# Optimization experiments

Measured on AMD Instinct MI355X. Metric: run time of the kernel, lower is better.

The kernel has to match this reference:

```python
import jax, jax.numpy as jnp
import numpy as np

EPS = 1e-5  # torch BatchNorm1d / LayerNorm default eps
B, S, CTX, C, H = 64, 31, 2048, 512, 8  # S must be num_particles+1 = 31
DH = C // H


def layernorm(x, g, b):
    mu = x.mean(-1, keepdims=True)
    var = x.var(-1, keepdims=True)
    return (x - mu) / jnp.sqrt(var + EPS) * g + b


def setup_inputs() -> dict:
    key = jax.random.key(0)
    ks = jax.random.split(key, 16)
    w = lambda k, shape: jax.random.normal(k, shape, jnp.float32) * 0.02
    return {
        "queries": jax.random.normal(ks[0], (B, S, C), jnp.float32),
        "contexts": jax.random.normal(ks[1], (B, CTX, C), jnp.float32),
        # SelfAttention params (BatchNorm1d(C) in training mode, q/k/v no bias, out with bias)
        "sa_bn_g": jnp.ones((C,), jnp.float32),
        "sa_bn_b": jnp.zeros((C,), jnp.float32),
        "sa_q_w": w(ks[2], (C, C)),
        "sa_k_w": w(ks[3], (C, C)),
        "sa_v_w": w(ks[4], (C, C)),
        "sa_out_w": w(ks[5], (C, C)),
        "sa_out_b": jnp.zeros((C,), jnp.float32),
        "sa_pre_g": jnp.ones((S * S,), jnp.float32),  # BatchNorm1d(961) on energy
        "sa_pre_b": jnp.zeros((S * S,), jnp.float32),
        # Cross Attention params (LayerNorm on queries, q/k/v no bias, out with bias)
        "ca_ln_g": jnp.ones((C,), jnp.float32),
        "ca_ln_b": jnp.zeros((C,), jnp.float32),
        "ca_q_w": w(ks[6], (C, C)),
        "ca_k_w": w(ks[7], (C, C)),
        "ca_v_w": w(ks[8], (C, C)),
        "ca_out_w": w(ks[9], (C, C)),
        "ca_out_b": jnp.zeros((C,), jnp.float32),
        # FFN: LN -> SiLU -> Linear(C,2C,no bias) -> LN -> SiLU -> Linear(2C,C,no bias)
        "ff_ln1_g": jnp.ones((C,), jnp.float32),
        "ff_ln1_b": jnp.zeros((C,), jnp.float32),
        "ff_w1": w(ks[10], (2 * C, C)),
        "ff_ln2_g": jnp.ones((2 * C,), jnp.float32),
        "ff_ln2_b": jnp.zeros((2 * C,), jnp.float32),
        "ff_w2": w(ks[11], (C, 2 * C)),
    }


def reference(queries, contexts, sa_bn_g, sa_bn_b, sa_q_w, sa_k_w, sa_v_w,
              sa_out_w, sa_out_b, sa_pre_g, sa_pre_b, ca_ln_g, ca_ln_b,
              ca_q_w, ca_k_w, ca_v_w, ca_out_w, ca_out_b, ff_ln1_g, ff_ln1_b,
              ff_w1, ff_ln2_g, ff_ln2_b, ff_w2):
    scale = jnp.sqrt(jnp.asarray(C, queries.dtype))

    # ---- SelfAttention (normalization='Batch', training-mode batch stats) ----
    mu = queries.mean(axis=(0, 1))            # per-channel over (B, S)
    var = queries.var(axis=(0, 1))
    xn = (queries - mu) / jnp.sqrt(var + EPS) * sa_bn_g + sa_bn_b
    q = jnp.einsum('bsc,oc->bso', xn, sa_q_w).reshape(B, S, H, DH)
    k = jnp.einsum('bsc,oc->bso', xn, sa_k_w).reshape(B, S, H, DH)
    v = jnp.einsum('bsc,oc->bso', xn, sa_v_w).reshape(B, S, H, DH)
    energy = jnp.einsum('nqhc,nkhc->nhqk', q, k)          # (B,H,S,S)
    # pre-softmax BatchNorm1d over channels = flattened (q,k) positions, batch dims = (B, H)
    e = energy.reshape(B, H, S * S)                        # (B,H,S*S)
    mu2 = e.mean(axis=(0, 1))
    var2 = e.var(axis=(0, 1))
    en = (e - mu2) / jnp.sqrt(var2 + EPS) * sa_pre_g + sa_pre_b
    energy_post = en.reshape(B, H, S, S)
    attn = jax.nn.softmax(energy_post / scale, axis=-1)
    o = jnp.einsum('nhql,nlhc->nqhc', attn, v).reshape(B, S, C)
    o = jnp.einsum('bsc,oc->bso', o, sa_out_w) + sa_out_b
    x_sa = o + queries                                     # residual

    # ---- Cross Attention (LayerNorm on queries pre-projection) ----
    qn = layernorm(x_sa, ca_ln_g, ca_ln_b)
    q2 = jnp.einsum('bsc,oc->bso', qn, ca_q_w).reshape(B, S, H, DH)
    k2 = jnp.einsum('btc,oc->bto', contexts, ca_k_w).reshape(B, CTX, H, DH)
    v2 = jnp.einsum('btc,oc->bto', contexts, ca_v_w).reshape(B, CTX, H, DH)
    energy2 = jnp.einsum('nqhc,nkhc->nhqk', q2, k2)        # (B,H,S,CTX)
    attn2 = jax.nn.softmax(energy2 / scale, axis=-1)
    o2 = jnp.einsum('nhql,nlhc->nqhc', attn2, v2).reshape(B, S, C)
    o2 = jnp.einsum('bsc,oc->bso', o2, ca_out_w) + ca_out_b
    x_ca = o2 + x_sa                                       # residual (queries_pre)

    # ---- FFN: LN -> SiLU -> Linear -> LN -> SiLU -> Linear, + residual ----
    h = jax.nn.silu(layernorm(x_ca, ff_ln1_g, ff_ln1_b))
    h = jnp.einsum('bsc,oc->bso', h, ff_w1)                # (B,S,2C)
    h = jax.nn.silu(layernorm(h, ff_ln2_g, ff_ln2_b))
    h = jnp.einsum('bsc,oc->bso', h, ff_w2)                # (B,S,C)
    out = x_ca + h                                         # dropout p=0.0 -> identity
    return out, energy2
```

## Files before the change

### kernel.cpp

```cpp
#include <hip/hip_runtime.h>
#include <hip/hip_bf16.h>
#include <cstdint>
#include <cstddef>

using u16 = unsigned short;
typedef short short8 __attribute__((ext_vector_type(8)));
typedef short short4v __attribute__((ext_vector_type(4)));
typedef float f32x4  __attribute__((ext_vector_type(4)));

#define DEV static __device__ __forceinline__

DEV float b2f(u16 u){ union{ unsigned i; float f; } v; v.i = ((unsigned)u)<<16; return v.f; }
DEV u16 f2b(float f){
  unsigned i = __builtin_bit_cast(unsigned, f);
  unsigned r = (i + 0x7FFFu + ((i>>16)&1u)) >> 16;
  return (u16)r;
}
DEV f32x4 mfma16(short8 a, short8 b, f32x4 c){
  return __builtin_amdgcn_mfma_f32_16x16x32_bf16(a, b, c, 0, 0, 0);
}

constexpr int Bn=64, Sn=31, Tn=2048, Cn=512, Hn=8;
constexpr int Rn=Bn*Sn;
constexpr int BHn=Bn*Hn;
constexpr int HRn=Hn*Sn;
constexpr float EPSf=1e-5f;
constexpr float INV_SCALE=0.04419417382415922f;

__global__ void k_badorder(float* out){
  if(threadIdx.x==0) out[0]=2000.f;
}

__global__ __launch_bounds__(256) void k_cvt(const float* __restrict__ in,
    u16* __restrict__ out, int n8){
  int i = blockIdx.x*256 + threadIdx.x;
  if(i>=n8) return;
  f32x4 a=*(const f32x4*)&in[(size_t)i*8];
  f32x4 b=*(const f32x4*)&in[(size_t)i*8+4];
  short8 o;
  #pragma unroll
  for(int j=0;j<4;++j){ o[j]=(short)f2b(a[j]); o[4+j]=(short)f2b(b[j]); }
  *(short8*)&out[(size_t)i*8]=o;
}

__global__ __launch_bounds__(256) void k_bn1_partial(const float* __restrict__ q,
    float* __restrict__ ps, float* __restrict__ psq){
  int c = blockIdx.x*256 + threadIdx.x;
  int r0 = blockIdx.y*124;
  float s=0.f, sq=0.f;
  for(int r=r0; r<r0+124; ++r){ float v=q[(size_t)r*Cn+c]; s+=v; sq+=v*v; }
  ps [blockIdx.y*Cn+c]=s;
  psq[blockIdx.y*Cn+c]=sq;
}
__global__ __launch_bounds__(512) void k_bn1_final(const float* __restrict__ ps,
    const float* __restrict__ psq, float* __restrict__ mu, float* __restrict__ rstd){
  int c = threadIdx.x;
  float s=0.f, sq=0.f;
  for(int i=0;i<16;++i){ s+=ps[i*Cn+c]; sq+=psq[i*Cn+c]; }
  float m = s/(float)Rn;
  float v = sq/(float)Rn - m*m;
  mu[c]=m; rstd[c]=rsqrtf(v+EPSf);
}
__global__ __launch_bounds__(256) void k_bn1_apply(const float* __restrict__ q,
    const float* __restrict__ mu, const float* __restrict__ rstd,
    const float* __restrict__ g, const float* __restrict__ b, u16* __restrict__ xn){
  int idx = blockIdx.x*256 + threadIdx.x;
  int row = idx>>6; int c0 = (idx&63)*8;
  f32x4 x0=*(const f32x4*)&q[(size_t)row*Cn + c0];
  f32x4 x1=*(const f32x4*)&q[(size_t)row*Cn + c0 + 4];
  short8 o;
  #pragma unroll
  for(int j=0;j<4;++j){
    int c=c0+j;
    o[j]  =(short)f2b((x0[j]-mu[c  ])*rstd[c  ]*g[c  ]+b[c  ]);
    o[4+j]=(short)f2b((x1[j]-mu[c+4])*rstd[c+4]*g[c+4]+b[c+4]);
  }
  *(short8*)&xn[(size_t)row*Cn + c0] = o;
}

template<bool F32OUT, bool RES32>
__global__ __launch_bounds__(256) void k_gemm64(
    const u16* __restrict__ A, const u16* __restrict__ W,
    const float* __restrict__ bias, const void* __restrict__ res,
    void* __restrict__ outv, int M, int N, int K)
{
  __shared__ u16 As[64][72];
  __shared__ u16 Ws[64][72];
  const int t=threadIdx.x, w=t>>6, l=t&63;
  const int m0=blockIdx.x*64, n0=blockIdx.y*64;
  const int lr=l&15, lk=(l>>4)*8;
  f32x4 zero={0.f,0.f,0.f,0.f};
  f32x4 acc[4];
  #pragma unroll
  for(int i=0;i<4;++i) acc[i]=zero;
  const int row0=t>>3, c8=(t&7)*8;
  for(int k0=0;k0<K;k0+=64){
    short8 a0=*(const short8*)&A[(size_t)(m0+row0   )*K + k0 + c8];
    short8 a1=*(const short8*)&A[(size_t)(m0+32+row0)*K + k0 + c8];
    short8 w0=*(const short8*)&W[(size_t)(n0+row0   )*K + k0 + c8];
    short8 w1=*(const short8*)&W[(size_t)(n0+32+row0)*K + k0 + c8];
    __syncthreads();
    *(short8*)&As[row0   ][c8]=a0;
    *(short8*)&As[32+row0][c8]=a1;
    *(short8*)&Ws[row0   ][c8]=w0;
    *(short8*)&Ws[32+row0][c8]=w1;
    __syncthreads();
    #pragma unroll
    for(int ks=0;ks<64;ks+=32){
      short8 af=*(const short8*)&As[w*16+lr][ks+lk];
      #pragma unroll
      for(int nf=0;nf<4;++nf){
        short8 bf=*(const short8*)&Ws[nf*16+lr][ks+lk];
        acc[nf]=mfma16(af,bf,acc[nf]);
      }
    }
  }
  const int r0=w*16+(l>>4)*4;
  #pragma unroll
  for(int nf=0;nf<4;++nf){
    const int n=n0+nf*16+lr;
    float bv = bias? bias[n] : 0.f;
    #pragma unroll
    for(int r=0;r<4;++r){
      const int m=m0+r0+r;
      float vv=acc[nf][r]+bv;
      if(res){
        if(RES32) vv += ((const float*)res)[(size_t)m*N+n];
        else      vv += b2f(((const u16*)res)[(size_t)m*N+n]);
      }
      if(F32OUT) ((float*)outv)[(size_t)m*N+n]=vv;
      else       ((u16*)outv)[(size_t)m*N+n]=f2b(vv);
    }
  }
}

__global__ __launch_bounds__(64) void k_energy1(const u16* __restrict__ q,
    const u16* __restrict__ k, float* __restrict__ e1){
  __shared__ u16 qs[32][72];
  __shared__ u16 ks_[32][72];
  const int bh=blockIdx.x, b=bh>>3, h=bh&7;
  const int t=threadIdx.x, l=t;
  #pragma unroll
  for(int i=0;i<4;++i){
    int flat=i*64+t; int row=flat>>3, c8=(flat&7)*8;
    short8 zq={0,0,0,0,0,0,0,0}, zk={0,0,0,0,0,0,0,0};
    if(row<31){
      zq=*(const short8*)&q[(size_t)(b*31+row)*Cn + h*64 + c8];
      zk=*(const short8*)&k[(size_t)(b*31+row)*Cn + h*64 + c8];
    }
    *(short8*)&qs [row][c8]=zq;
    *(short8*)&ks_[row][c8]=zk;
  }
  __syncthreads();
  const int lr=l&15, lk=(l>>4)*8;
  f32x4 zero={0.f,0.f,0.f,0.f};
  f32x4 acc[2][2];
  acc[0][0]=zero; acc[0][1]=zero; acc[1][0]=zero; acc[1][1]=zero;
  #pragma unroll
  for(int ks=0;ks<64;ks+=32){
    short8 a0=*(const short8*)&qs [lr   ][ks+lk];
    short8 a1=*(const short8*)&qs [16+lr][ks+lk];
    short8 b0=*(const short8*)&ks_[lr   ][ks+lk];
    short8 b1=*(const short8*)&ks_[16+lr][ks+lk];
    acc[0][0]=mfma16(a0,b0,acc[0][0]);
    acc[0][1]=mfma16(a0,b1,acc[0][1]);
    acc[1][0]=mfma16(a1,b0,acc[1][0]);
    acc[1][1]=mfma16(a1,b1,acc[1][1]);
  }
  const int r0=(l>>4)*4;
  #pragma unroll
  for(int i=0;i<2;++i)
    #pragma unroll
    for(int j=0;j<2;++j)
      #pragma unroll
      for(int r=0;r<4;++r){
        int qi=i*16+r0+r, ki=j*16+lr;
        if(qi<31 && ki<31) e1[(size_t)bh*961 + qi*31 + ki]=acc[i][j][r];
      }
}

__global__ __launch_bounds__(256) void k_bn2_partial(const float* __restrict__ e1,
    float* __restrict__ ps, float* __restrict__ psq){
  int p=blockIdx.x*256+threadIdx.x;
  if(p>=961) return;
  int r0=blockIdx.y*64;
  float s=0.f, sq=0.f;
  for(int r=r0;r<r0+64;++r){ float v=e1[(size_t)r*961+p]; s+=v; sq+=v*v; }
  ps [blockIdx.y*961+p]=s;
  psq[blockIdx.y*961+p]=sq;
}
__global__ __launch_bounds__(1024) void k_bn2_final(const float* __restrict__ ps,
    const float* __restrict__ psq, float* __restrict__ mu2, float* __restrict__ rstd2){
  int p=threadIdx.x; if(p>=961) return;
  float s=0.f, sq=0.f;
  for(int i=0;i<8;++i){ s+=ps[i*961+p]; sq+=psq[i*961+p]; }
  float m=s/512.f, v=sq/512.f-m*m;
  mu2[p]=m; rstd2[p]=rsqrtf(v+EPSf);
}

__global__ __launch_bounds__(256) void k_softmax_sa(const float* __restrict__ e1,
    const float* __restrict__ mu2, const float* __restrict__ rstd2,
    const float* __restrict__ g2, const float* __restrict__ bb2, u16* __restrict__ attn){
  int gidx=blockIdx.x*256+threadIdx.x;
  int bh=gidx/31, qi=gidx-bh*31;
  const float* er = e1 + (size_t)bh*961 + qi*31;
  float lg[31]; float mx=-1e30f;
  #pragma unroll
  for(int kk=0;kk<31;++kk){
    int p=qi*31+kk;
    float en=(er[kk]-mu2[p])*rstd2[p]*g2[p]+bb2[p];
    lg[kk]=en*INV_SCALE;
    mx=fmaxf(mx,lg[kk]);
  }
  float s=0.f;
  #pragma unroll
  for(int kk=0;kk<31;++kk){ lg[kk]=expf(lg[kk]-mx); s+=lg[kk]; }
  float inv=1.f/s;
  u16* ar = attn + (size_t)bh*1024 + qi*32;
  #pragma unroll
  for(int kk=0;kk<31;++kk) ar[kk]=f2b(lg[kk]*inv);
  ar[31]=0;
}

__global__ __launch_bounds__(64) void k_pv_sa(const u16* __restrict__ attn,
    const u16* __restrict__ v, u16* __restrict__ o1){
  __shared__ u16 vs[64][40];
  const int bh=blockIdx.x, b=bh>>3, h=bh&7;
  const int l=threadIdx.x;
  for(int kv=0;kv<31;++kv) vs[l][kv]=v[(size_t)(b*31+kv)*Cn + h*64 + l];
  vs[l][31]=0;
  __syncthreads();
  const int lr=l&15, lk=(l>>4)*8;
  f32x4 zero={0.f,0.f,0.f,0.f};
  f32x4 acc[2][4];
  #pragma unroll
  for(int i=0;i<2;++i)
    #pragma unroll
    for(int nf=0;nf<4;++nf) acc[i][nf]=zero;
  short8 a0=*(const short8*)&attn[(size_t)bh*1024 + lr*32 + lk];
  short8 a1=*(const short8*)&attn[(size_t)bh*1024 + (16+lr)*32 + lk];
  #pragma unroll
  for(int nf=0;nf<4;++nf){
    short8 bf=*(const short8*)&vs[nf*16+lr][lk];
    acc[0][nf]=mfma16(a0,bf,acc[0][nf]);
    acc[1][nf]=mfma16(a1,bf,acc[1][nf]);
  }
  const int r0=(l>>4)*4;
  #pragma unroll
  for(int i=0;i<2;++i)
    #pragma unroll
    for(int nf=0;nf<4;++nf)
      #pragma unroll
      for(int r=0;r<4;++r){
        int qi=i*16+r0+r;
        if(qi<31){
          int dh=nf*16+lr;
          o1[(size_t)(b*31+qi)*Cn + h*64 + dh]=f2b(acc[i][nf][r]);
        }
      }
}

template<int Wd, bool SILU>
__global__ __launch_bounds__(256) void k_ln(const u16* __restrict__ x,
    const float* __restrict__ g, const float* __restrict__ b, u16* __restrict__ out){
  const int w=threadIdx.x>>6, l=threadIdx.x&63;
  const int row=blockIdx.x*4+w;
  constexpr int NC=Wd/512;
  float v[NC*8];
  #pragma unroll
  for(int i=0;i<NC;++i){
    short8 s=*(const short8*)&x[(size_t)row*Wd + i*512 + l*8];
    #pragma unroll
    for(int j=0;j<8;++j) v[i*8+j]=b2f((u16)s[j]);
  }
  float s1=0.f, s2=0.f;
  #pragma unroll
  for(int e=0;e<NC*8;++e){ s1+=v[e]; s2+=v[e]*v[e]; }
  #pragma unroll
  for(int off=1;off<64;off<<=1){ s1+=__shfl_xor(s1,off,64); s2+=__shfl_xor(s2,off,64); }
  float m=s1/(float)Wd, var=s2/(float)Wd-m*m, rs=rsqrtf(var+EPSf);
  #pragma unroll
  for(int i=0;i<NC;++i){
    short8 o;
    #pragma unroll
    for(int j=0;j<8;++j){
      int c=i*512+l*8+j;
      float y=(v[i*8+j]-m)*rs*g[c]+b[c];
      if(SILU) y=y/(1.f+expf(-y));
      o[j]=(short)f2b(y);
    }
    *(short8*)&out[(size_t)row*Wd + i*512 + l*8]=o;
  }
}

__global__ __launch_bounds__(256) void k_qk(const u16* __restrict__ q2,
    const float* __restrict__ Wk, u16* __restrict__ qk){
  __shared__ u16 qs[32][72];
  __shared__ u16 bt[128][72];
  const int bh=blockIdx.x, b=bh>>3, h=bh&7;
  const int t=threadIdx.x, w=t>>6, l=t&63;
  {
    int row=t>>3, c8=(t&7)*8;
    short8 z={0,0,0,0,0,0,0,0};
    if(row<31) z=*(const short8*)&q2[(size_t)(b*31+row)*Cn + h*64 + c8];
    *(short8*)&qs[row][c8]=z;
  }
  const int lr=l&15, lk=(l>>4)*8;
  const int r0=(l>>4)*4;
  for(int nc=0;nc<512;nc+=128){
    __syncthreads();
    #pragma unroll
    for(int i=0;i<8;++i){
      int g=i*256+t;
      int d=g>>5, c4=(g&31)*4;
      f32x4 v=*(const f32x4*)&Wk[(size_t)(h*64+d)*Cn + nc + c4];
      #pragma unroll
      for(int jj=0;jj<4;++jj) bt[c4+jj][d]=f2b(v[jj]);
    }
    __syncthreads();
    f32x4 zero={0.f,0.f,0.f,0.f};
    f32x4 acc[2][2];
    acc[0][0]=zero; acc[0][1]=zero; acc[1][0]=zero; acc[1][1]=zero;
    #pragma unroll
    for(int ks=0;ks<64;ks+=32){
      short8 a0=*(const short8*)&qs[lr   ][ks+lk];
      short8 a1=*(const short8*)&qs[16+lr][ks+lk];
      #pragma unroll
      for(int nf=0;nf<2;++nf){
        short8 bf=*(const short8*)&bt[w*32+nf*16+lr][ks+lk];
        acc[0][nf]=mfma16(a0,bf,acc[0][nf]);
        acc[1][nf]=mfma16(a1,bf,acc[1][nf]);
      }
    }
    #pragma unroll
    for(int i=0;i<2;++i)
      #pragma unroll
      for(int nf=0;nf<2;++nf)
        #pragma unroll
        for(int r=0;r<4;++r){
          int qi=i*16+r0+r;
          if(qi<31)
            qk[((size_t)b*HRn + h*31 + qi)*Cn + nc + w*32 + nf*16 + lr]=f2b(acc[i][nf][r]);
        }
  }
}

__global__ __launch_bounds__(512) void k_e2big(const u16* __restrict__ qk,
    const float* __restrict__ ctx, float* __restrict__ e2){
  __shared__ u16 As[256][72];
  __shared__ u16 Bs[128][72];
  const int tb=blockIdx.x*128, b=blockIdx.y;
  const int t=threadIdx.x, w=t>>6, l=t&63;
  const int lr=l&15, lk=(l>>4)*8;
  const int wr=(w>>1)*64, wc=(w&1)*64;
  f32x4 zero={0.f,0.f,0.f,0.f};
  f32x4 acc[4][4];
  #pragma unroll
  for(int i=0;i<4;++i)
    #pragma unroll
    for(int j=0;j<4;++j) acc[i][j]=zero;
  for(int k0=0;k0<512;k0+=64){
    __syncthreads();
    #pragma unroll
    for(int i=0;i<4;++i){
      int g=i*512+t; int row=g>>3, c8=(g&7)*8;
      short8 z={0,0,0,0,0,0,0,0};
      if(row<HRn) z=*(const short8*)&qk[((size_t)b*HRn+row)*Cn + k0 + c8];
      *(short8*)&As[row][c8]=z;
    }
    #pragma unroll
    for(int i=0;i<4;++i){
      int g=i*512+t; int row=g>>4, c4=(g&15)*4;
      f32x4 v=*(const f32x4*)&ctx[((size_t)b*Tn + tb + row)*Cn + k0 + c4];
      short4v o;
      #pragma unroll
      for(int jj=0;jj<4;++jj) o[jj]=(short)f2b(v[jj]);
      *(short4v*)&Bs[row][c4]=o;
    }
    __syncthreads();
    #pragma unroll
    for(int ks=0;ks<64;ks+=32){
      short8 af[4], bf[4];
      #pragma unroll
      for(int i=0;i<4;++i){
        af[i]=*(const short8*)&As[wr+i*16+lr][ks+lk];
        bf[i]=*(const short8*)&Bs[wc+i*16+lr][ks+lk];
      }
      #pragma unroll
      for(int i=0;i<4;++i)
        #pragma unroll
        for(int j=0;j<4;++j)
          acc[i][j]=mfma16(af[i],bf[j],acc[i][j]);
    }
  }
  const int r0=(l>>4)*4;
  #pragma unroll
  for(int i=0;i<4;++i)
    #pragma unroll
    for(int j=0;j<4;++j)
      #pragma unroll
      for(int r=0;r<4;++r){
        int rm=wr+i*16+r0+r;
        if(rm<HRn)
          e2[((size_t)b*HRn+rm)*Tn + tb + wc + j*16 + lr]=acc[i][j][r];
      }
}

__global__ __launch_bounds__(256) void k_pstats(const float* __restrict__ e2,
    u16* __restrict__ pb, float* __restrict__ st){
  const int w=threadIdx.x>>6, l=threadIdx.x&63;
  const int gi=blockIdx.x*4+w;
  const int b=gi>>8, m=gi&255;
  u16* pr = pb + ((size_t)b*256+m)*2048;
  if(m>=HRn){
    short8 z={0,0,0,0,0,0,0,0};
    #pragma unroll
    for(int i=0;i<4;++i) *(short8*)&pr[i*512 + l*8]=z;
    return;
  }
  const float* er = e2 + ((size_t)b*HRn+m)*Tn;
  float v[32];
  #pragma unroll
  for(int i=0;i<4;++i){
    f32x4 a=*(const f32x4*)&er[i*512 + l*8];
    f32x4 c=*(const f32x4*)&er[i*512 + l*8 + 4];
    #pragma unroll
    for(int j=0;j<4;++j){ v[i*8+j]=a[j]*INV_SCALE; v[i*8+4+j]=c[j]*INV_SCALE; }
  }
  float mx=v[0];
  #pragma unroll
  for(int e=1;e<32;++e) mx=fmaxf(mx,v[e]);
  #pragma unroll
  for(int off=1;off<64;off<<=1) mx=fmaxf(mx,__shfl_xor(mx,off,64));
  float s=0.f;
  #pragma unroll
  for(int e=0;e<32;++e){ v[e]=expf(v[e]-mx); s+=v[e]; }
  #pragma unroll
  for(int off=1;off<64;off<<=1) s+=__shfl_xor(s,off,64);
  #pragma unroll
  for(int i=0;i<4;++i){
    short8 o;
    #pragma unroll
    for(int j=0;j<8;++j) o[j]=(short)f2b(v[i*8+j]);
    *(short8*)&pr[i*512 + l*8]=o;
  }
  if(l==0){ st[2*((size_t)b*HRn+m)]=mx; st[2*((size_t)b*HRn+m)+1]=s; }
}

__global__ __launch_bounds__(512) void k_pv2(const u16* __restrict__ pb,
    const float* __restrict__ ctx, const float* __restrict__ st,
    u16* __restrict__ o2t){
  __shared__ u16 As[128][72];
  __shared__ u16 Bs[128][76];
  const int n0=blockIdx.x*128, m0=blockIdx.y*128, b=blockIdx.z;
  const int t=threadIdx.x, w=t>>6, l=t&63;
  const int lr=l&15, lk=(l>>4)*8;
  const int wm=(w>>2)*64, wn=(w&3)*32;
  f32x4 zero={0.f,0.f,0.f,0.f};
  f32x4 acc[4][2];
  #pragma unroll
  for(int i=0;i<4;++i){ acc[i][0]=zero; acc[i][1]=zero; }
  const int arow=t>>3, ac8=(t&7)*8;
  const int bc=t&127, bq=(t>>7)*4;
  for(int kb=0;kb<Tn;kb+=64){
    __syncthreads();
    #pragma unroll
    for(int i=0;i<2;++i){
      int row=arow+i*64;
      *(short8*)&As[row][ac8] =
        *(const short8*)&pb[((size_t)b*256 + m0 + row)*Tn + kb + ac8];
    }
    #pragma unroll
    for(int i=0;i<4;++i){
      int kt0=(bq+i)*4;
      short4v o;
      #pragma unroll
      for(int jj=0;jj<4;++jj)
        o[jj]=(short)f2b(ctx[((size_t)b*Tn + kb + kt0 + jj)*Cn + n0 + bc]);
      *(short4v*)&Bs[bc][kt0]=o;
    }
    __syncthreads();
    #pragma unroll
    for(int ks=0;ks<64;ks+=32){
      short8 af[4], bf[2];
      #pragma unroll
      for(int i=0;i<4;++i)
        af[i]=*(const short8*)&As[wm+i*16+lr][ks+lk];
      #pragma unroll
      for(int j=0;j<2;++j){
        const u16* p=&Bs[wn+j*16+lr][ks+lk];
        short4v lo=*(const short4v*)p;
        short4v hi=*(const short4v*)(p+4);
        short8 bb;
        #pragma unroll
        for(int jj=0;jj<4;++jj){ bb[jj]=lo[jj]; bb[4+jj]=hi[jj]; }
        bf[j]=bb;
      }
      #pragma unroll
      for(int i=0;i<4;++i)
        #pragma unroll
        for(int j=0;j<2;++j)
          acc[i][j]=mfma16(af[i],bf[j],acc[i][j]);
    }
  }
  const int r0=(l>>4)*4;
  #pragma unroll
  for(int i=0;i<4;++i)
    #pragma unroll
    for(int j=0;j<2;++j)
      #pragma unroll
      for(int r=0;r<4;++r){
        int rm=m0+wm+i*16+r0+r;
        if(rm<HRn){
          float inv=1.f/st[2*((size_t)b*HRn+rm)+1];
          o2t[((size_t)b*HRn+rm)*Cn + n0+wn+j*16+lr]=f2b(acc[i][j][r]*inv);
        }
      }
}

__global__ __launch_bounds__(256) void k_o2proj(const u16* __restrict__ o2t,
    const float* __restrict__ Wv, u16* __restrict__ o2b){
  __shared__ u16 As[32][72];
  __shared__ u16 Ws[64][72];
  const int bh=blockIdx.x, b=bh>>3, h=bh&7;
  const int t=threadIdx.x, w=t>>6, l=t&63;
  const int lr=l&15, lk=(l>>4)*8;
  f32x4 zero={0.f,0.f,0.f,0.f};
  f32x4 acc[2]; acc[0]=zero; acc[1]=zero;
  for(int k0=0;k0<512;k0+=64){
    __syncthreads();
    {
      int row=t>>3, c8=(t&7)*8;
      short8 z={0,0,0,0,0,0,0,0};
      if(row<31) z=*(const short8*)&o2t[((size_t)b*HRn + h*31 + row)*Cn + k0 + c8];
      *(short8*)&As[row][c8]=z;
    }
    #pragma unroll
    for(int i=0;i<4;++i){
      int g=i*256+t; int row=g>>4, c4=(g&15)*4;
      f32x4 v=*(const f32x4*)&Wv[(size_t)(h*64+row)*Cn + k0 + c4];
      short4v o;
      #pragma unroll
      for(int jj=0;jj<4;++jj) o[jj]=(short)f2b(v[jj]);
      *(short4v*)&Ws[row][c4]=o;
    }
    __syncthreads();
    #pragma unroll
    for(int ks=0;ks<64;ks+=32){
      short8 a0=*(const short8*)&As[lr   ][ks+lk];
      short8 a1=*(const short8*)&As[16+lr][ks+lk];
      short8 bf=*(const short8*)&Ws[w*16+lr][ks+lk];
      acc[0]=mfma16(a0,bf,acc[0]);
      acc[1]=mfma16(a1,bf,acc[1]);
    }
  }
  const int r0=(l>>4)*4;
  #pragma unroll
  for(int i=0;i<2;++i)
    #pragma unroll
    for(int r=0;r<4;++r){
      int qi=i*16+r0+r;
      if(qi<31)
        o2b[((size_t)b*31+qi)*Cn + h*64 + w*16 + lr]=f2b(acc[i][r]);
    }
}

extern "C" void kernel_launch(void* const* d_in, const int* in_sizes, int n_in,
                              void* d_out, int out_size, void* d_ws, size_t ws_size,
                              hipStream_t stream){
  (void)out_size; (void)ws_size;
  float* outp=(float*)d_out;
  float* e2  =outp + (size_t)Rn*Cn;
  if(n_in<24 || in_sizes[0]!=Rn*Cn || in_sizes[1]!=Bn*Tn*Cn ||
     in_sizes[4]!=Cn*Cn || in_sizes[9]!=961 || in_sizes[20]!=2*Cn*Cn){
    k_badorder<<<1,64,0,stream>>>(outp);
    return;
  }
  const float* queries =(const float*)d_in[0];
  const float* contexts=(const float*)d_in[1];
  const float* sa_bn_g =(const float*)d_in[2];
  const float* sa_bn_b =(const float*)d_in[3];
  const float* sa_q_w  =(const float*)d_in[4];
  const float* sa_k_w  =(const float*)d_in[5];
  const float* sa_v_w  =(const float*)d_in[6];
  const float* sa_out_w=(const float*)d_in[7];
  const float* sa_out_b=(const float*)d_in[8];
  const float* sa_pre_g=(const float*)d_in[9];
  const float* sa_pre_b=(const float*)d_in[10];
  const float* ca_ln_g =(const float*)d_in[11];
  const float* ca_ln_b =(const float*)d_in[12];
  const float* ca_q_w  =(const float*)d_in[13];
  const float* ca_k_w  =(const float*)d_in[14];
  const float* ca_v_w  =(const float*)d_in[15];
  const float* ca_out_w=(const float*)d_in[16];
  const float* ca_out_b=(const float*)d_in[17];
  const float* ff_ln1_g=(const float*)d_in[18];
  const float* ff_ln1_b=(const float*)d_in[19];
  const float* ff_w1   =(const float*)d_in[20];
  const float* ff_ln2_g=(const float*)d_in[21];
  const float* ff_ln2_b=(const float*)d_in[22];
  const float* ff_w2   =(const float*)d_in[23];

  char* ws=(char*)d_ws;
  size_t off=0;
  auto alloc=[&](size_t bytes)->char*{
    char* p=ws+off; off=(off+bytes+255)&~(size_t)255; return p;
  };
  float* ps1  =(float*)alloc(16*Cn*4);
  float* psq1 =(float*)alloc(16*Cn*4);
  float* mu1  =(float*)alloc(Cn*4);
  float* rstd1=(float*)alloc(Cn*4);
  u16* w_sq=(u16*)alloc((size_t)Cn*Cn*2);
  u16* w_sk=(u16*)alloc((size_t)Cn*Cn*2);
  u16* w_sv=(u16*)alloc((size_t)Cn*Cn*2);
  u16* w_so=(u16*)alloc((size_t)Cn*Cn*2);
  u16* w_cq=(u16*)alloc((size_t)Cn*Cn*2);
  u16* w_co=(u16*)alloc((size_t)Cn*Cn*2);
  u16* w_f1=(u16*)alloc((size_t)2*Cn*Cn*2);
  u16* w_f2=(u16*)alloc((size_t)2*Cn*Cn*2);
  u16* xn  =(u16*)alloc((size_t)Rn*Cn*2);
  u16* qb  =(u16*)alloc((size_t)Rn*Cn*2);
  u16* kb  =(u16*)alloc((size_t)Rn*Cn*2);
  u16* vb  =(u16*)alloc((size_t)Rn*Cn*2);
  float* e1  =(float*)alloc((size_t)BHn*961*4);
  float* ps2 =(float*)alloc(8*961*4);
  float* psq2=(float*)alloc(8*961*4);
  float* mu2 =(float*)alloc(961*4);
  float* rstd2=(float*)alloc(961*4);
  u16* attn1=(u16*)alloc((size_t)BHn*1024*2);
  u16* o1  =(u16*)alloc((size_t)Rn*Cn*2);
  u16* xsa =(u16*)alloc((size_t)Rn*Cn*2);
  u16* qn  =(u16*)alloc((size_t)Rn*Cn*2);
  u16* q2b =(u16*)alloc((size_t)Rn*Cn*2);
  u16* qk  =(u16*)alloc((size_t)Bn*HRn*Cn*2);
  float* st=(float*)alloc((size_t)BHn*31*2*4);
  u16* o2b =(u16*)alloc((size_t)Rn*Cn*2);
  u16* xca =(u16*)alloc((size_t)Rn*Cn*2);
  u16* pb  =(u16*)alloc((size_t)Bn*256*Tn*2);
  u16* o2t = qk;
  u16* f1  = xn;
  u16* t1  = qb;
  u16* f2  = vb;

  dim3 blk256(256), blk64(64), blk512(512);
  dim3 g64(Rn/64, Cn/64);

  k_cvt<<<Cn*Cn/2048, blk256,0,stream>>>(sa_q_w, w_sq, Cn*Cn/8);
  k_cvt<<<Cn*Cn/2048, blk256,0,stream>>>(sa_k_w, w_sk, Cn*Cn/8);
  k_cvt<<<Cn*Cn/2048, blk256,0,stream>>>(sa_v_w, w_sv, Cn*Cn/8);
  k_cvt<<<Cn*Cn/2048, blk256,0,stream>>>(sa_out_w, w_so, Cn*Cn/8);
  k_cvt<<<Cn*Cn/2048, blk256,0,stream>>>(ca_q_w, w_cq, Cn*Cn/8);
  k_cvt<<<Cn*Cn/2048, blk256,0,stream>>>(ca_out_w, w_co, Cn*Cn/8);
  k_cvt<<<2*Cn*Cn/2048, blk256,0,stream>>>(ff_w1, w_f1, 2*Cn*Cn/8);
  k_cvt<<<2*Cn*Cn/2048, blk256,0,stream>>>(ff_w2, w_f2, 2*Cn*Cn/8);

  k_bn1_partial<<<dim3(2,16),blk256,0,stream>>>(queries, ps1, psq1);
  k_bn1_final<<<1,512,0,stream>>>(ps1,psq1,mu1,rstd1);
  k_bn1_apply<<<Rn*Cn/(256*8),blk256,0,stream>>>(queries,mu1,rstd1,sa_bn_g,sa_bn_b,xn);
  k_gemm64<false,false><<<g64,blk256,0,stream>>>(xn,w_sq,nullptr,nullptr,qb,Rn,Cn,Cn);
  k_gemm64<false,false><<<g64,blk256,0,stream>>>(xn,w_sk,nullptr,nullptr,kb,Rn,Cn,Cn);
  k_gemm64<false,false><<<g64,blk256,0,stream>>>(xn,w_sv,nullptr,nullptr,vb,Rn,Cn,Cn);
  k_energy1<<<BHn,blk64,0,stream>>>(qb,kb,e1);
  k_bn2_partial<<<dim3(4,8),blk256,0,stream>>>(e1,ps2,psq2);
  k_bn2_final<<<1,1024,0,stream>>>(ps2,psq2,mu2,rstd2);
  k_softmax_sa<<<62,blk256,0,stream>>>(e1,mu2,rstd2,sa_pre_g,sa_pre_b,attn1);
  k_pv_sa<<<BHn,blk64,0,stream>>>(attn1,vb,o1);
  k_gemm64<false,true><<<g64,blk256,0,stream>>>(o1,w_so,sa_out_b,queries,xsa,Rn,Cn,Cn);

  k_ln<512,false><<<Rn/4,blk256,0,stream>>>(xsa,ca_ln_g,ca_ln_b,qn);
  k_gemm64<false,false><<<g64,blk256,0,stream>>>(qn,w_cq,nullptr,nullptr,q2b,Rn,Cn,Cn);
  k_qk<<<BHn,blk256,0,stream>>>(q2b,ca_k_w,qk);
  k_e2big<<<dim3(Tn/128,Bn),blk512,0,stream>>>(qk,contexts,e2);
  k_pstats<<<Bn*256/4,blk256,0,stream>>>(e2,pb,st);
  k_pv2<<<dim3(Cn/128,2,Bn),blk512,0,stream>>>(pb,contexts,st,o2t);
  k_o2proj<<<BHn,blk256,0,stream>>>(o2t,ca_v_w,o2b);
  k_gemm64<false,false><<<g64,blk256,0,stream>>>(o2b,w_co,ca_out_b,xsa,xca,Rn,Cn,Cn);

  k_ln<512,true><<<Rn/4,blk256,0,stream>>>(xca,ff_ln1_g,ff_ln1_b,f1);
  k_gemm64<false,false><<<dim3(Rn/64,1024/64),blk256,0,stream>>>(f1,w_f1,nullptr,nullptr,t1,Rn,1024,Cn);
  k_ln<1024,true><<<Rn/4,blk256,0,stream>>>(t1,ff_ln2_g,ff_ln2_b,f2);
  k_gemm64<true,false><<<g64,blk256,0,stream>>>(f2,w_f2,nullptr,xca,outp,Rn,Cn,1024);
}
```

Baseline: 442.1 us.

## Batch weight casts, fuse BN-apply into QKV GEMM, cache bf16 contexts

```diff
diff --git a/kernel.cpp b/kernel.cpp
--- a/kernel.cpp
+++ b/kernel.cpp
@@ -31,16 +31,19 @@
   if(threadIdx.x==0) out[0]=2000.f;
 }
 
-__global__ __launch_bounds__(256) void k_cvt(const float* __restrict__ in,
-    u16* __restrict__ out, int n8){
+struct Src8 { const float* p[8]; };
+__global__ __launch_bounds__(256) void k_cvtall(Src8 s, u16* __restrict__ dst){
   int i = blockIdx.x*256 + threadIdx.x;
-  if(i>=n8) return;
-  f32x4 a=*(const f32x4*)&in[(size_t)i*8];
-  f32x4 b=*(const f32x4*)&in[(size_t)i*8+4];
+  int seg, j=i;
+  if(j>=196608){ if(j>=262144){seg=7;j-=262144;} else {seg=6;j-=196608;} }
+  else { seg=j>>15; j&=32767; }
+  const float* src=s.p[seg];
+  f32x4 a=*(const f32x4*)&src[(size_t)j*8];
+  f32x4 b=*(const f32x4*)&src[(size_t)j*8+4];
   short8 o;
   #pragma unroll
-  for(int j=0;j<4;++j){ o[j]=(short)f2b(a[j]); o[4+j]=(short)f2b(b[j]); }
-  *(short8*)&out[(size_t)i*8]=o;
+  for(int q=0;q<4;++q){ o[q]=(short)f2b(a[q]); o[4+q]=(short)f2b(b[q]); }
+  *(short8*)&dst[(size_t)i*8]=o;
 }
 
 __global__ __launch_bounds__(256) void k_bn1_partial(const float* __restrict__ q,
@@ -53,29 +56,80 @@
   psq[blockIdx.y*Cn+c]=sq;
 }
 __global__ __launch_bounds__(512) void k_bn1_final(const float* __restrict__ ps,
-    const float* __restrict__ psq, float* __restrict__ mu, float* __restrict__ rstd){
+    const float* __restrict__ psq, const float* __restrict__ g,
+    const float* __restrict__ b, float* __restrict__ scale, float* __restrict__ shift){
   int c = threadIdx.x;
   float s=0.f, sq=0.f;
   for(int i=0;i<16;++i){ s+=ps[i*Cn+c]; sq+=psq[i*Cn+c]; }
   float m = s/(float)Rn;
   float v = sq/(float)Rn - m*m;
-  mu[c]=m; rstd[c]=rsqrtf(v+EPSf);
-}
-__global__ __launch_bounds__(256) void k_bn1_apply(const float* __restrict__ q,
-    const float* __restrict__ mu, const float* __restrict__ rstd,
-    const float* __restrict__ g, const float* __restrict__ b, u16* __restrict__ xn){
-  int idx = blockIdx.x*256 + threadIdx.x;
-  int row = idx>>6; int c0 = (idx&63)*8;
-  f32x4 x0=*(const f32x4*)&q[(size_t)row*Cn + c0];
-  f32x4 x1=*(const f32x4*)&q[(size_t)row*Cn + c0 + 4];
-  short8 o;
-  #pragma unroll
-  for(int j=0;j<4;++j){
-    int c=c0+j;
-    o[j]  =(short)f2b((x0[j]-mu[c  ])*rstd[c  ]*g[c  ]+b[c  ]);
-    o[4+j]=(short)f2b((x1[j]-mu[c+4])*rstd[c+4]*g[c+4]+b[c+4]);
-  }
-  *(short8*)&xn[(size_t)row*Cn + c0] = o;
+  float rs = rsqrtf(v+EPSf);
+  float sc = rs*g[c];
+  scale[c]=sc; shift[c]=b[c]-m*sc;
+}
+
+__global__ __launch_bounds__(256) void k_qkv(
+    const float* __restrict__ q, const float* __restrict__ scale,
+    const float* __restrict__ shift,
+    const u16* __restrict__ W0, const u16* __restrict__ W1, const u16* __restrict__ W2,
+    u16* __restrict__ o0, u16* __restrict__ o1v, u16* __restrict__ o2v)
+{
+  __shared__ u16 As[64][72];
+  __shared__ u16 Ws[64][72];
+  const int z=blockIdx.z;
+  const u16* W = (z==0)?W0:((z==1)?W1:W2);
+  u16* out     = (z==0)?o0:((z==1)?o1v:o2v);
+  const int t=threadIdx.x, w=t>>6, l=t&63;
+  const int m0=blockIdx.x*64, n0=blockIdx.y*64;
+  const int lr=l&15, lk=(l>>4)*8;
+  f32x4 zero={0.f,0.f,0.f,0.f};
+  f32x4 acc[4];
+  #pragma unroll
+  for(int i=0;i<4;++i) acc[i]=zero;
+  const int row0=t>>3, c8=(t&7)*8;
+  for(int k0=0;k0<Cn;k0+=64){
+    f32x4 sc0=*(const f32x4*)&scale[k0+c8], sc1=*(const f32x4*)&scale[k0+c8+4];
+    f32x4 sh0=*(const f32x4*)&shift[k0+c8], sh1=*(const f32x4*)&shift[k0+c8+4];
+    f32x4 x00=*(const f32x4*)&q[(size_t)(m0+row0   )*Cn+k0+c8];
+    f32x4 x01=*(const f32x4*)&q[(size_t)(m0+row0   )*Cn+k0+c8+4];
+    f32x4 x10=*(const f32x4*)&q[(size_t)(m0+32+row0)*Cn+k0+c8];
+    f32x4 x11=*(const f32x4*)&q[(size_t)(m0+32+row0)*Cn+k0+c8+4];
+    short8 a0,a1;
+    #pragma unroll
+    for(int j=0;j<4;++j){
+      a0[j]  =(short)f2b(fmaf(x00[j],sc0[j],sh0[j]));
+      a0[4+j]=(short)f2b(fmaf(x01[j],sc1[j],sh1[j]));
+      a1[j]  =(short)f2b(fmaf(x10[j],sc0[j],sh0[j]));
+      a1[4+j]=(short)f2b(fmaf(x11[j],sc1[j],sh1[j]));
+    }
+    short8 w0=*(const short8*)&W[(size_t)(n0+row0   )*Cn + k0 + c8];
+    short8 w1=*(const short8*)&W[(size_t)(n0+32+row0)*Cn + k0 + c8];
+    __syncthreads();
+    *(short8*)&As[row0   ][c8]=a0;
+    *(short8*)&As[32+row0][c8]=a1;
+    *(short8*)&Ws[row0   ][c8]=w0;
+    *(short8*)&Ws[32+row0][c8]=w1;
+    __syncthreads();
+    #pragma unroll
+    for(int ks=0;ks<64;ks+=32){
+      short8 af=*(const short8*)&As[w*16+lr][ks+lk];
+      #pragma unroll
+      for(int nf=0;nf<4;++nf){
+        short8 bf=*(const short8*)&Ws[nf*16+lr][ks+lk];
+        acc[nf]=mfma16(af,bf,acc[nf]);
+      }
+    }
+  }
+  const int r0=w*16+(l>>4)*4;
+  #pragma unroll
+  for(int nf=0;nf<4;++nf){
+    const int n=n0+nf*16+lr;
+    #pragma unroll
+    for(int r=0;r<4;++r){
+      const int m=m0+r0+r;
+      out[(size_t)m*Cn+n]=f2b(acc[nf][r]);
+    }
+  }
 }
 
 template<bool F32OUT, bool RES32>
@@ -346,7 +400,7 @@
 }
 
 __global__ __launch_bounds__(512) void k_e2big(const u16* __restrict__ qk,
-    const float* __restrict__ ctx, float* __restrict__ e2){
+    const float* __restrict__ ctx, float* __restrict__ e2, u16* __restrict__ ctxb){
   __shared__ u16 As[256][72];
   __shared__ u16 Bs[128][72];
   const int tb=blockIdx.x*128, b=blockIdx.y;
@@ -376,6 +430,7 @@
       #pragma unroll
       for(int jj=0;jj<4;++jj) o[jj]=(short)f2b(v[jj]);
       *(short4v*)&Bs[row][c4]=o;
+      *(short4v*)&ctxb[((size_t)b*Tn + tb + row)*Cn + k0 + c4]=o;
     }
     __syncthreads();
     #pragma unroll
@@ -448,7 +503,7 @@
 }
 
 __global__ __launch_bounds__(512) void k_pv2(const u16* __restrict__ pb,
-    const float* __restrict__ ctx, const float* __restrict__ st,
+    const u16* __restrict__ ctxb, const float* __restrict__ st,
     u16* __restrict__ o2t){
   __shared__ u16 As[128][72];
   __shared__ u16 Bs[128][76];
@@ -476,7 +531,7 @@
       short4v o;
       #pragma unroll
       for(int jj=0;jj<4;++jj)
-        o[jj]=(short)f2b(ctx[((size_t)b*Tn + kb + kt0 + jj)*Cn + n0 + bc]);
+        o[jj]=(short)ctxb[((size_t)b*Tn + kb + kt0 + jj)*Cn + n0 + bc];
       *(short4v*)&Bs[bc][kt0]=o;
     }
     __syncthreads();
@@ -608,8 +663,8 @@
   };
   float* ps1  =(float*)alloc(16*Cn*4);
   float* psq1 =(float*)alloc(16*Cn*4);
-  float* mu1  =(float*)alloc(Cn*4);
-  float* rstd1=(float*)alloc(Cn*4);
+  float* scale1=(float*)alloc(Cn*4);
+  float* shift1=(float*)alloc(Cn*4);
   u16* w_sq=(u16*)alloc((size_t)Cn*Cn*2);
   u16* w_sk=(u16*)alloc((size_t)Cn*Cn*2);
   u16* w_sv=(u16*)alloc((size_t)Cn*Cn*2);
@@ -618,7 +673,6 @@
   u16* w_co=(u16*)alloc((size_t)Cn*Cn*2);
   u16* w_f1=(u16*)alloc((size_t)2*Cn*Cn*2);
   u16* w_f2=(u16*)alloc((size_t)2*Cn*Cn*2);
-  u16* xn  =(u16*)alloc((size_t)Rn*Cn*2);
   u16* qb  =(u16*)alloc((size_t)Rn*Cn*2);
   u16* kb  =(u16*)alloc((size_t)Rn*Cn*2);
   u16* vb  =(u16*)alloc((size_t)Rn*Cn*2);
@@ -637,29 +691,22 @@
   u16* o2b =(u16*)alloc((size_t)Rn*Cn*2);
   u16* xca =(u16*)alloc((size_t)Rn*Cn*2);
   u16* pb  =(u16*)alloc((size_t)Bn*256*Tn*2);
+  u16* ctxb=(u16*)alloc((size_t)Bn*Tn*Cn*2);
   u16* o2t = qk;
-  u16* f1  = xn;
+  u16* f1  = o1;
   u16* t1  = qb;
   u16* f2  = vb;
 
   dim3 blk256(256), blk64(64), blk512(512);
   dim3 g64(Rn/64, Cn/64);
 
-  k_cvt<<<Cn*Cn/2048, blk256,0,stream>>>(sa_q_w, w_sq, Cn*Cn/8);
-  k_cvt<<<Cn*Cn/2048, blk256,0,stream>>>(sa_k_w, w_sk, Cn*Cn/8);
-  k_cvt<<<Cn*Cn/2048, blk256,0,stream>>>(sa_v_w, w_sv, Cn*Cn/8);
-  k_cvt<<<Cn*Cn/2048, blk256,0,stream>>>(sa_out_w, w_so, Cn*Cn/8);
-  k_cvt<<<Cn*Cn/2048, blk256,0,stream>>>(ca_q_w, w_cq, Cn*Cn/8);
-  k_cvt<<<Cn*Cn/2048, blk256,0,stream>>>(ca_out_w, w_co, Cn*Cn/8);
-  k_cvt<<<2*Cn*Cn/2048, blk256,0,stream>>>(ff_w1, w_f1, 2*Cn*Cn/8);
-  k_cvt<<<2*Cn*Cn/2048, blk256,0,stream>>>(ff_w2, w_f2, 2*Cn*Cn/8);
+  Src8 s8; s8.p[0]=sa_q_w; s8.p[1]=sa_k_w; s8.p[2]=sa_v_w; s8.p[3]=sa_out_w;
+  s8.p[4]=ca_q_w; s8.p[5]=ca_out_w; s8.p[6]=ff_w1; s8.p[7]=ff_w2;
+  k_cvtall<<<1280,blk256,0,stream>>>(s8, w_sq);
 
   k_bn1_partial<<<dim3(2,16),blk256,0,stream>>>(queries, ps1, psq1);
-  k_bn1_final<<<1,512,0,stream>>>(ps1,psq1,mu1,rstd1);
-  k_bn1_apply<<<Rn*Cn/(256*8),blk256,0,stream>>>(queries,mu1,rstd1,sa_bn_g,sa_bn_b,xn);
-  k_gemm64<false,false><<<g64,blk256,0,stream>>>(xn,w_sq,nullptr,nullptr,qb,Rn,Cn,Cn);
-  k_gemm64<false,false><<<g64,blk256,0,stream>>>(xn,w_sk,nullptr,nullptr,kb,Rn,Cn,Cn);
-  k_gemm64<false,false><<<g64,blk256,0,stream>>>(xn,w_sv,nullptr,nullptr,vb,Rn,Cn,Cn);
+  k_bn1_final<<<1,512,0,stream>>>(ps1,psq1,sa_bn_g,sa_bn_b,scale1,shift1);
+  k_qkv<<<dim3(31,8,3),blk256,0,stream>>>(queries,scale1,shift1,w_sq,w_sk,w_sv,qb,kb,vb);
   k_energy1<<<BHn,blk64,0,stream>>>(qb,kb,e1);
   k_bn2_partial<<<dim3(4,8),blk256,0,stream>>>(e1,ps2,psq2);
   k_bn2_final<<<1,1024,0,stream>>>(ps2,psq2,mu2,rstd2);
@@ -670,9 +717,9 @@
   k_ln<512,false><<<Rn/4,blk256,0,stream>>>(xsa,ca_ln_g,ca_ln_b,qn);
   k_gemm64<false,false><<<g64,blk256,0,stream>>>(qn,w_cq,nullptr,nullptr,q2b,Rn,Cn,Cn);
   k_qk<<<BHn,blk256,0,stream>>>(q2b,ca_k_w,qk);
-  k_e2big<<<dim3(Tn/128,Bn),blk512,0,stream>>>(qk,contexts,e2);
+  k_e2big<<<dim3(Tn/128,Bn),blk512,0,stream>>>(qk,contexts,e2,ctxb);
   k_pstats<<<Bn*256/4,blk256,0,stream>>>(e2,pb,st);
-  k_pv2<<<dim3(Cn/128,2,Bn),blk512,0,stream>>>(pb,contexts,st,o2t);
+  k_pv2<<<dim3(Cn/128,2,Bn),blk512,0,stream>>>(pb,ctxb,st,o2t);
   k_o2proj<<<BHn,blk256,0,stream>>>(o2t,ca_v_w,o2b);
   k_gemm64<false,false><<<g64,blk256,0,stream>>>(o2b,w_co,ca_out_b,xsa,xca,Rn,Cn,Cn);
 
```

New measurement: 424.6 us. -4.0%, faster.
